# Kernel optimization log

Hardware: AMD Instinct MI355X
Metric: run time of the kernel (lower is better)

Reference implementation:

```python
import jax, jax.numpy as jnp
import numpy as np

POOL, D_MODEL, D_FF, M_DIM = 512, 1024, 4096, 64
B, S, K = 2, 2048, 8


def setup_inputs() -> dict:
    key = jax.random.key(0)
    ks = jax.random.split(key, 8)
    x = jax.random.normal(ks[0], (B, S, D_MODEL), dtype=jnp.float32)
    selected_indices = jax.random.randint(ks[1], (B, S, K), 0, POOL, dtype=jnp.int32)
    pattern_weights = jax.random.normal(ks[2], (B, S, K), dtype=jnp.float32)
    base_patterns = 0.02 * jax.random.normal(ks[3], (POOL, D_FF), dtype=jnp.float32)
    # nn.Linear(d_model, pool_size*mod_dim): weight [P*M, d_model], xavier-uniform
    lim_cm = float(np.sqrt(6.0 / (D_MODEL + POOL * M_DIM)))
    cm_w = jax.random.uniform(ks[4], (POOL * M_DIM, D_MODEL), jnp.float32, -lim_cm, lim_cm)
    cm_b = jnp.zeros((POOL * M_DIM,), jnp.float32)
    adj_proj = 0.01 * jax.random.normal(ks[5], (M_DIM, D_FF), dtype=jnp.float32)
    lim_w2 = float(np.sqrt(6.0 / (D_FF + D_MODEL)))
    w2_w = jax.random.uniform(ks[6], (D_MODEL, D_FF), jnp.float32, -lim_w2, lim_w2)
    w2_b = jnp.zeros((D_MODEL,), jnp.float32)
    return {"x": x, "selected_indices": selected_indices, "pattern_weights": pattern_weights,
            "base_patterns": base_patterns, "cm_w": cm_w, "cm_b": cm_b,
            "adj_proj": adj_proj, "w2_w": w2_w, "w2_b": w2_b}


def reference(x, selected_indices, pattern_weights, base_patterns, cm_w, cm_b, adj_proj, w2_w, w2_b):
    b, s, k = selected_indices.shape
    # gather base firing patterns for selected neurons: [b,s,k,d_ff]
    bp = base_patterns[selected_indices]
    # dense context modulation then gather (matches original module): [b,s,P,M]
    mod = (jnp.einsum('bsd,nd->bsn', x, cm_w) + cm_b).reshape(b, s, POOL, M_DIM)
    sel_mod = jnp.take_along_axis(mod, selected_indices[..., None], axis=2)  # [b,s,k,M]
    adjustments = jnp.einsum('bskm,mf->bskf', sel_mod, adj_proj)
    adjusted = bp + adjustments  # [b,s,k,d_ff]
    w = jax.nn.softmax(pattern_weights, axis=-1)
    combined = jnp.einsum('bsk,bskf->bsf', w, adjusted)  # [b,s,d_ff]
    activated = jax.nn.gelu(combined, approximate=False)  # torch default gelu = exact erf
    return jnp.einsum('bsf,df->bsd', activated, w2_w) + w2_b
```

## Files before the change

### kernel.cpp

```cpp
#include <hip/hip_runtime.h>
#include <math.h>

#define T_    4096
#define K_    8
#define POOL_ 512
#define DM_   1024
#define DFF_  4096
#define MD_   64
#define KC_   576
#define NSPLIT 4
#define NCAP  256

typedef __bf16 bf16x8 __attribute__((ext_vector_type(8)));
typedef __bf16 bf16x4 __attribute__((ext_vector_type(4)));
typedef float  f32x4  __attribute__((ext_vector_type(4)));

typedef __attribute__((address_space(1))) const void g_void;
typedef __attribute__((address_space(3))) void s_void;

__device__ __forceinline__ void async_ld16(const void* g, void* s) {
    __builtin_amdgcn_global_load_lds((g_void*)g, (s_void*)s, 16, 0, 0);
}
__device__ __forceinline__ float gelu_exact(float g) {
    return 0.5f * g * (1.f + erff(g * 0.70710678118654752f));
}
__device__ __forceinline__ bf16x4 cvt4(float4 v) {
    bf16x4 o;
    o[0] = (__bf16)v.x; o[1] = (__bf16)v.y; o[2] = (__bf16)v.z; o[3] = (__bf16)v.w;
    return o;
}

__global__ __launch_bounds__(256) void k_hist(const int* __restrict__ sel,
                                              int* __restrict__ counts) {
    int i = blockIdx.x * 256 + threadIdx.x;
    if (i < T_ * K_) atomicAdd(&counts[sel[i]], 1);
}

__global__ __launch_bounds__(512) void k_scan(const int* __restrict__ counts,
                                              int* __restrict__ offsets,
                                              int* __restrict__ cursor) {
    __shared__ int s[512];
    const int t = threadIdx.x;
    const int c = counts[t];
    s[t] = c;
    __syncthreads();
    for (int d = 1; d < 512; d <<= 1) {
        int v = (t >= d) ? s[t - d] : 0;
        __syncthreads();
        s[t] += v;
        __syncthreads();
    }
    offsets[t] = s[t] - c;
    cursor[t]  = s[t] - c;
    if (t == 511) offsets[512] = s[511];
}

__global__ __launch_bounds__(256) void k_scatter(const int* __restrict__ sel,
                                                 int* __restrict__ cursor,
                                                 int* __restrict__ bucket,
                                                 int* __restrict__ rank) {
    int i = blockIdx.x * 256 + threadIdx.x;
    if (i < T_ * K_) {
        int p = sel[i];
        int pos = atomicAdd(&cursor[p], 1);
        bucket[pos] = i;
        rank[i] = pos;
    }
}

__global__ __launch_bounds__(256, 8) void k_selmod(
    const float* __restrict__ x, const float* __restrict__ cm_w,
    const int* __restrict__ bucket, const int* __restrict__ offsets,
    float* __restrict__ Yp)
{
    const int p     = blockIdx.x;
    const int slice = blockIdx.y;
    const int tid   = threadIdx.x;
    __shared__ int list[NCAP];
    __shared__ __align__(16) __bf16 Xl[64][72];
    __shared__ __align__(16) __bf16 Wl[64][72];

    const int off = offsets[p];
    const int n   = min(offsets[p + 1] - off, NCAP);
    if (n == 0) return;
    for (int i = tid; i < n; i += 256) list[i] = bucket[off + i] >> 3;
    __syncthreads();

    const int wave = tid >> 6, lane = tid & 63, quad = lane >> 4, l15 = lane & 15;
    const int srow = tid >> 3;
    const int part = tid & 7;
    const int k0   = slice * (DM_ / NSPLIT);

    const float* w0 = cm_w + (long)(p * 64 + srow)      * DM_ + k0;
    const float* w1 = cm_w + (long)(p * 64 + srow + 32) * DM_ + k0;
    float* Yo = Yp + (long)slice * ((long)T_ * K_ * MD_);

    for (int base = 0; base < n; base += 64) {
        f32x4 acc[4] = {};
        int li0 = base + srow;      if (li0 >= n) li0 = n - 1;
        int li1 = base + srow + 32; if (li1 >= n) li1 = n - 1;
        const float* x0 = x + (long)list[li0] * DM_ + k0;
        const float* x1 = x + (long)list[li1] * DM_ + k0;

        for (int kc = 0; kc < DM_ / NSPLIT; kc += 64) {
            #pragma unroll
            for (int u = 0; u < 2; ++u) {
                const int c = kc + u * 32 + part * 4;
                float4 a0 = *(const float4*)(x0 + c);
                float4 a1 = *(const float4*)(x1 + c);
                float4 b0 = *(const float4*)(w0 + c);
                float4 b1 = *(const float4*)(w1 + c);
                const int lc = u * 32 + part * 4;
                *(bf16x4*)&Xl[srow     ][lc] = cvt4(a0);
                *(bf16x4*)&Xl[srow + 32][lc] = cvt4(a1);
                *(bf16x4*)&Wl[srow     ][lc] = cvt4(b0);
                *(bf16x4*)&Wl[srow + 32][lc] = cvt4(b1);
            }
            __syncthreads();
            #pragma unroll
            for (int ks = 0; ks < 2; ++ks) {
                const int ko = ks * 32 + quad * 8;
                bf16x8 bfr = *(const bf16x8*)&Wl[wave * 16 + l15][ko];
                #pragma unroll
                for (int i = 0; i < 4; ++i) {
                    bf16x8 afr = *(const bf16x8*)&Xl[i * 16 + l15][ko];
                    acc[i] = __builtin_amdgcn_mfma_f32_16x16x32_bf16(afr, bfr, acc[i], 0, 0, 0);
                }
            }
            __syncthreads();
        }
        const int mcol = wave * 16 + l15;
        #pragma unroll
        for (int i = 0; i < 4; ++i) {
            #pragma unroll
            for (int r = 0; r < 4; ++r) {
                int prow = base + i * 16 + quad * 4 + r;
                if (prow < n)
                    Yo[(long)(off + prow) * MD_ + mcol] = acc[i][r];
            }
        }
    }
}

__global__ __launch_bounds__(256) void k_wdense(
    const float* __restrict__ Yp, const int* __restrict__ sel,
    const int* __restrict__ rank, const float* __restrict__ pw,
    const float* __restrict__ cm_b, __bf16* __restrict__ Wd)
{
    const int tid = threadIdx.x;
    const int tt = tid >> 6, m = tid & 63;
    const int t = blockIdx.x * 4 + tt;
    __shared__ float w_s[4][8];
    __shared__ int   sidx[4][8];
    __shared__ int   rnk[4][8];
    __shared__ __align__(16) __bf16 row[4][KC_];

    if (m < 8) {
        w_s[tt][m]  = pw[t * 8 + m];
        sidx[tt][m] = sel[t * 8 + m];
        rnk[tt][m]  = rank[t * 8 + m];
    }
    __syncthreads();
    if (m == 0) {
        float mx = w_s[tt][0];
        #pragma unroll
        for (int k = 1; k < 8; ++k) mx = fmaxf(mx, w_s[tt][k]);
        float sum = 0.f;
        #pragma unroll
        for (int k = 0; k < 8; ++k) { float e = expf(w_s[tt][k] - mx); w_s[tt][k] = e; sum += e; }
        float inv = 1.f / sum;
        #pragma unroll
        for (int k = 0; k < 8; ++k) w_s[tt][k] *= inv;
    }
    __syncthreads();
    *(uint4*)&row[tt][m * 8] = make_uint4(0, 0, 0, 0);
    {
        const long YN = (long)T_ * K_ * MD_;
        float a = 0.f;
        #pragma unroll
        for (int k = 0; k < 8; ++k) {
            const long base = (long)rnk[tt][k] * MD_ + m;
            float y = cm_b[sidx[tt][k] * 64 + m];
            #pragma unroll
            for (int s = 0; s < NSPLIT; ++s) y += Yp[s * YN + base];
            a += w_s[tt][k] * y;
        }
        row[tt][512 + m] = (__bf16)a;
    }
    __syncthreads();
    if (m == 0) {
        #pragma unroll
        for (int k = 0; k < 8; ++k) {
            int c = sidx[tt][k];
            row[tt][c] = (__bf16)((float)row[tt][c] + w_s[tt][k]);
        }
    }
    __syncthreads();
    const uint4* src = (const uint4*)&row[0][0];
    uint4* dst = (uint4*)(Wd + (long)blockIdx.x * 4 * KC_);
    for (int e = tid; e < 4 * KC_ * 2 / 16; e += 256) dst[e] = src[e];
}

__global__ __launch_bounds__(256) void k_buildP(
    const float* __restrict__ bp, const float* __restrict__ adj,
    __bf16* __restrict__ P)
{
    __shared__ __bf16 tile[64][72];
    const int tid = threadIdx.x;
    const int bx = blockIdx.x, f0 = blockIdx.y * 64;
    const float* src = (bx < 8) ? (bp + (long)bx * 64 * DFF_) : adj;
    for (int e = tid; e < 4096; e += 256) {
        int f = e & 63, c = e >> 6;
        tile[c][f] = (__bf16)src[(long)c * DFF_ + f0 + f];
    }
    __syncthreads();
    const int c0 = bx * 64;
    for (int e = tid; e < 4096; e += 256) {
        int c = e & 63, f = e >> 6;
        P[(long)(f0 + f) * KC_ + c0 + c] = tile[c][f];
    }
}

__global__ __launch_bounds__(256) void k_cvt(const float* __restrict__ src,
                                             __bf16* __restrict__ dst, int n16) {
    int i = blockIdx.x * 256 + threadIdx.x;
    if (i >= n16) return;
    const float4* s = (const float4*)src + (long)i * 4;
    float4 a = s[0], b = s[1], c = s[2], d = s[3];
    bf16x8 o0, o1;
    o0[0]=(__bf16)a.x; o0[1]=(__bf16)a.y; o0[2]=(__bf16)a.z; o0[3]=(__bf16)a.w;
    o0[4]=(__bf16)b.x; o0[5]=(__bf16)b.y; o0[6]=(__bf16)b.z; o0[7]=(__bf16)b.w;
    o1[0]=(__bf16)c.x; o1[1]=(__bf16)c.y; o1[2]=(__bf16)c.z; o1[3]=(__bf16)c.w;
    o1[4]=(__bf16)d.x; o1[5]=(__bf16)d.y; o1[6]=(__bf16)d.z; o1[7]=(__bf16)d.w;
    bf16x8* dp = (bf16x8*)dst + (long)i * 2;
    dp[0] = o0; dp[1] = o1;
}

__global__ __launch_bounds__(256) void k_actgemm(
    const __bf16* __restrict__ A, const __bf16* __restrict__ Bw,
    __bf16* __restrict__ act)
{
    __shared__ __align__(16) __bf16 sA[128 * 32];
    __shared__ __align__(16) __bf16 sB[128 * 32];
    const int tid  = threadIdx.x;
    const int tm   = blockIdx.y * 128, tn = blockIdx.x * 128;
    const int wave = tid >> 6, lane = tid & 63, quad = lane >> 4, l15 = lane & 15;
    const int wm   = (wave >> 1) * 64, wn = (wave & 1) * 64;

    f32x4 acc[4][4] = {};

    const int e    = tid * 8;
    const int srow = e >> 5;
    const int scol = e & 31;
    const __bf16* agp0 = A  + ((long)(tm + srow)      * KC_ + scol);
    const __bf16* agp1 = A  + ((long)(tm + 64 + srow) * KC_ + scol);
    const __bf16* bgp0 = Bw + ((long)(tn + srow)      * KC_ + scol);
    const __bf16* bgp1 = Bw + ((long)(tn + 64 + srow) * KC_ + scol);
    void* sa0 = (void*)(sA + e);
    void* sa1 = (void*)(sA + 2048 + e);
    void* sb0 = (void*)(sB + e);
    void* sb1 = (void*)(sB + 2048 + e);

    for (int kk = 0; kk < KC_; kk += 32) {
        async_ld16(agp0 + kk, sa0);
        async_ld16(agp1 + kk, sa1);
        async_ld16(bgp0 + kk, sb0);
        async_ld16(bgp1 + kk, sb1);
        __syncthreads();
        bf16x8 af[4], bf[4];
        #pragma unroll
        for (int i = 0; i < 4; ++i)
            af[i] = *(const bf16x8*)(sA + (wm + i * 16 + l15) * 32 + quad * 8);
        #pragma unroll
        for (int j = 0; j < 4; ++j)
            bf[j] = *(const bf16x8*)(sB + (wn + j * 16 + l15) * 32 + quad * 8);
        #pragma unroll
        for (int i = 0; i < 4; ++i)
            #pragma unroll
            for (int j = 0; j < 4; ++j)
                acc[i][j] = __builtin_amdgcn_mfma_f32_16x16x32_bf16(af[i], bf[j], acc[i][j], 0, 0, 0);
        __syncthreads();
    }

    #pragma unroll
    for (int j = 0; j < 4; ++j) {
        const int col = tn + wn + j * 16 + l15;
        #pragma unroll
        for (int i = 0; i < 4; ++i) {
            const int row = tm + wm + i * 16 + quad * 4;
            #pragma unroll
            for (int r = 0; r < 4; ++r)
                act[(long)(row + r) * DFF_ + col] = (__bf16)gelu_exact(acc[i][j][r]);
        }
    }
}

__global__ __launch_bounds__(256) void k_outgemm(
    const __bf16* __restrict__ A, const __bf16* __restrict__ Bw,
    const float* __restrict__ bias, float* __restrict__ out)
{
    __shared__ __align__(16) __bf16 sA[128 * 128];
    __shared__ __align__(16) __bf16 sB[128 * 128];
    const int tid  = threadIdx.x;
    const int tm   = blockIdx.y * 128, tn = blockIdx.x * 128;
    const int wave = tid >> 6, lane = tid & 63, quad = lane >> 4, l15 = lane & 15;
    const int wm   = (wave >> 1) * 64, wn = (wave & 1) * 64;

    f32x4 acc[4][4] = {};

    const int e  = tid * 8;
    const int r0 = e >> 5;
    const int cc = e & 31;

    for (int kk = 0; kk < DFF_; kk += 128) {
        #pragma unroll
        for (int s = 0; s < 4; ++s) {
            #pragma unroll
            for (int q = 0; q < 2; ++q) {
                async_ld16(A  + (long)(tm + q * 64 + r0) * DFF_ + kk + s * 32 + cc,
                           (void*)(sA + s * 4096 + q * 2048 + e));
                async_ld16(Bw + (long)(tn + q * 64 + r0) * DFF_ + kk + s * 32 + cc,
                           (void*)(sB + s * 4096 + q * 2048 + e));
            }
        }
        __syncthreads();
        #pragma unroll
        for (int s = 0; s < 4; ++s) {
            bf16x8 af[4], bf[4];
            #pragma unroll
            for (int i = 0; i < 4; ++i)
                af[i] = *(const bf16x8*)(sA + s * 4096 + (wm + i * 16 + l15) * 32 + quad * 8);
            #pragma unroll
            for (int j = 0; j < 4; ++j)
                bf[j] = *(const bf16x8*)(sB + s * 4096 + (wn + j * 16 + l15) * 32 + quad * 8);
            #pragma unroll
            for (int i = 0; i < 4; ++i)
                #pragma unroll
                for (int j = 0; j < 4; ++j)
                    acc[i][j] = __builtin_amdgcn_mfma_f32_16x16x32_bf16(af[i], bf[j], acc[i][j], 0, 0, 0);
        }
        __syncthreads();
    }

    #pragma unroll
    for (int j = 0; j < 4; ++j) {
        const int col = tn + wn + j * 16 + l15;
        const float bj = bias[col];
        #pragma unroll
        for (int i = 0; i < 4; ++i) {
            const int row = tm + wm + i * 16 + quad * 4;
            #pragma unroll
            for (int r = 0; r < 4; ++r)
                out[(long)(row + r) * 1024 + col] = acc[i][j][r] + bj;
        }
    }
}

extern "C" void kernel_launch(void* const* d_in, const int* in_sizes, int n_in,
                              void* d_out, int out_size, void* d_ws, size_t ws_size,
                              hipStream_t stream) {
    const float* x    = (const float*)d_in[0];
    const int*   sel  = (const int*)  d_in[1];
    const float* pw   = (const float*)d_in[2];
    const float* bp   = (const float*)d_in[3];
    const float* cm_w = (const float*)d_in[4];
    const float* cm_b = (const float*)d_in[5];
    const float* adj  = (const float*)d_in[6];
    const float* w2   = (const float*)d_in[7];
    const float* w2b  = (const float*)d_in[8];
    float* out = (float*)d_out;

    char* ws = (char*)d_ws;
    float*  Yp   = (float*)ws;
    __bf16* act  = (__bf16*)ws;
    __bf16* P    = (__bf16*)(ws + (size_t)32 * 1024 * 1024);
    __bf16* w2bf = (__bf16*)(ws + (size_t)37 * 1024 * 1024);
    char*  bins  = ws + (size_t)45 * 1024 * 1024;
    int* bucket  = (int*)bins;
    int* rank    = (int*)(bins + 131072);
    int* counts  = (int*)(bins + 262144);
    int* cursor  = (int*)(bins + 264192);
    int* offsets = (int*)(bins + 266240);

    __bf16* Wd = (__bf16*)d_out;

    hipMemsetAsync(counts, 0, 4096, stream);
    k_hist   <<<128, 256, 0, stream>>>(sel, counts);
    k_scan   <<<1,   512, 0, stream>>>(counts, offsets, cursor);
    k_scatter<<<128, 256, 0, stream>>>(sel, cursor, bucket, rank);
    k_selmod <<<dim3(POOL_, NSPLIT), 256, 0, stream>>>(x, cm_w, bucket, offsets, Yp);
    k_wdense <<<T_ / 4, 256, 0, stream>>>(Yp, sel, rank, pw, cm_b, Wd);
    k_buildP <<<dim3(9, 64), 256, 0, stream>>>(bp, adj, P);
    k_cvt    <<<1024, 256, 0, stream>>>(w2, w2bf, DM_ * DFF_ / 16);
    k_actgemm<<<dim3(DFF_ / 128, T_ / 128), 256, 0, stream>>>(Wd, P, act);
    k_outgemm<<<dim3(DM_ / 128, T_ / 128), 256, 0, stream>>>(act, w2bf, w2b, out);
}
```

Before: 417.5 us.

## Split selmod over output columns with full-K weight tile and prequantized bf16 x

Converts x to bf16 once in a separate pass, then restructures the context-modulation GEMM so each block owns 16 of the 64 output columns for a pool entry. The block caches that full 16x1024 weight slice in LDS and walks all of K, which removes the four-way K-split partial sums and their reduction in k_wdense. The intent is to cut fp32 x reads and the extra Yp traffic. The cost is an extra conversion kernel and each x row being gathered four times, once per column slice, and each block now does only one MFMA chain per k-step. Y now lives in the output buffer, and Wd is moved to an offset inside it.

```diff
diff --git a/kernel.cpp b/kernel.cpp
--- a/kernel.cpp
+++ b/kernel.cpp
@@ -8,7 +8,6 @@
 #define DFF_  4096
 #define MD_   64
 #define KC_   576
-#define NSPLIT 4
 #define NCAP  256
 
 typedef __bf16 bf16x8 __attribute__((ext_vector_type(8)));
@@ -65,159 +64,6 @@
         int pos = atomicAdd(&cursor[p], 1);
         bucket[pos] = i;
         rank[i] = pos;
-    }
-}
-
-__global__ __launch_bounds__(256, 8) void k_selmod(
-    const float* __restrict__ x, const float* __restrict__ cm_w,
-    const int* __restrict__ bucket, const int* __restrict__ offsets,
-    float* __restrict__ Yp)
-{
-    const int p     = blockIdx.x;
-    const int slice = blockIdx.y;
-    const int tid   = threadIdx.x;
-    __shared__ int list[NCAP];
-    __shared__ __align__(16) __bf16 Xl[64][72];
-    __shared__ __align__(16) __bf16 Wl[64][72];
-
-    const int off = offsets[p];
-    const int n   = min(offsets[p + 1] - off, NCAP);
-    if (n == 0) return;
-    for (int i = tid; i < n; i += 256) list[i] = bucket[off + i] >> 3;
-    __syncthreads();
-
-    const int wave = tid >> 6, lane = tid & 63, quad = lane >> 4, l15 = lane & 15;
-    const int srow = tid >> 3;
-    const int part = tid & 7;
-    const int k0   = slice * (DM_ / NSPLIT);
-
-    const float* w0 = cm_w + (long)(p * 64 + srow)      * DM_ + k0;
-    const float* w1 = cm_w + (long)(p * 64 + srow + 32) * DM_ + k0;
-    float* Yo = Yp + (long)slice * ((long)T_ * K_ * MD_);
-
-    for (int base = 0; base < n; base += 64) {
-        f32x4 acc[4] = {};
-        int li0 = base + srow;      if (li0 >= n) li0 = n - 1;
-        int li1 = base + srow + 32; if (li1 >= n) li1 = n - 1;
-        const float* x0 = x + (long)list[li0] * DM_ + k0;
-        const float* x1 = x + (long)list[li1] * DM_ + k0;
-
-        for (int kc = 0; kc < DM_ / NSPLIT; kc += 64) {
-            #pragma unroll
-            for (int u = 0; u < 2; ++u) {
-                const int c = kc + u * 32 + part * 4;
-                float4 a0 = *(const float4*)(x0 + c);
-                float4 a1 = *(const float4*)(x1 + c);
-                float4 b0 = *(const float4*)(w0 + c);
-                float4 b1 = *(const float4*)(w1 + c);
-                const int lc = u * 32 + part * 4;
-                *(bf16x4*)&Xl[srow     ][lc] = cvt4(a0);
-                *(bf16x4*)&Xl[srow + 32][lc] = cvt4(a1);
-                *(bf16x4*)&Wl[srow     ][lc] = cvt4(b0);
-                *(bf16x4*)&Wl[srow + 32][lc] = cvt4(b1);
-            }
-            __syncthreads();
-            #pragma unroll
-            for (int ks = 0; ks < 2; ++ks) {
-                const int ko = ks * 32 + quad * 8;
-                bf16x8 bfr = *(const bf16x8*)&Wl[wave * 16 + l15][ko];
-                #pragma unroll
-                for (int i = 0; i < 4; ++i) {
-                    bf16x8 afr = *(const bf16x8*)&Xl[i * 16 + l15][ko];
-                    acc[i] = __builtin_amdgcn_mfma_f32_16x16x32_bf16(afr, bfr, acc[i], 0, 0, 0);
-                }
-            }
-            __syncthreads();
-        }
-        const int mcol = wave * 16 + l15;
-        #pragma unroll
-        for (int i = 0; i < 4; ++i) {
-            #pragma unroll
-            for (int r = 0; r < 4; ++r) {
-                int prow = base + i * 16 + quad * 4 + r;
-                if (prow < n)
-                    Yo[(long)(off + prow) * MD_ + mcol] = acc[i][r];
-            }
-        }
-    }
-}
-
-__global__ __launch_bounds__(256) void k_wdense(
-    const float* __restrict__ Yp, const int* __restrict__ sel,
-    const int* __restrict__ rank, const float* __restrict__ pw,
-    const float* __restrict__ cm_b, __bf16* __restrict__ Wd)
-{
-    const int tid = threadIdx.x;
-    const int tt = tid >> 6, m = tid & 63;
-    const int t = blockIdx.x * 4 + tt;
-    __shared__ float w_s[4][8];
-    __shared__ int   sidx[4][8];
-    __shared__ int   rnk[4][8];
-    __shared__ __align__(16) __bf16 row[4][KC_];
-
-    if (m < 8) {
-        w_s[tt][m]  = pw[t * 8 + m];
-        sidx[tt][m] = sel[t * 8 + m];
-        rnk[tt][m]  = rank[t * 8 + m];
-    }
-    __syncthreads();
-    if (m == 0) {
-        float mx = w_s[tt][0];
-        #pragma unroll
-        for (int k = 1; k < 8; ++k) mx = fmaxf(mx, w_s[tt][k]);
-        float sum = 0.f;
-        #pragma unroll
-        for (int k = 0; k < 8; ++k) { float e = expf(w_s[tt][k] - mx); w_s[tt][k] = e; sum += e; }
-        float inv = 1.f / sum;
-        #pragma unroll
-        for (int k = 0; k < 8; ++k) w_s[tt][k] *= inv;
-    }
-    __syncthreads();
-    *(uint4*)&row[tt][m * 8] = make_uint4(0, 0, 0, 0);
-    {
-        const long YN = (long)T_ * K_ * MD_;
-        float a = 0.f;
-        #pragma unroll
-        for (int k = 0; k < 8; ++k) {
-            const long base = (long)rnk[tt][k] * MD_ + m;
-            float y = cm_b[sidx[tt][k] * 64 + m];
-            #pragma unroll
-            for (int s = 0; s < NSPLIT; ++s) y += Yp[s * YN + base];
-            a += w_s[tt][k] * y;
-        }
-        row[tt][512 + m] = (__bf16)a;
-    }
-    __syncthreads();
-    if (m == 0) {
-        #pragma unroll
-        for (int k = 0; k < 8; ++k) {
-            int c = sidx[tt][k];
-            row[tt][c] = (__bf16)((float)row[tt][c] + w_s[tt][k]);
-        }
-    }
-    __syncthreads();
-    const uint4* src = (const uint4*)&row[0][0];
-    uint4* dst = (uint4*)(Wd + (long)blockIdx.x * 4 * KC_);
-    for (int e = tid; e < 4 * KC_ * 2 / 16; e += 256) dst[e] = src[e];
-}
-
-__global__ __launch_bounds__(256) void k_buildP(
-    const float* __restrict__ bp, const float* __restrict__ adj,
-    __bf16* __restrict__ P)
-{
-    __shared__ __bf16 tile[64][72];
-    const int tid = threadIdx.x;
-    const int bx = blockIdx.x, f0 = blockIdx.y * 64;
-    const float* src = (bx < 8) ? (bp + (long)bx * 64 * DFF_) : adj;
-    for (int e = tid; e < 4096; e += 256) {
-        int f = e & 63, c = e >> 6;
-        tile[c][f] = (__bf16)src[(long)c * DFF_ + f0 + f];
-    }
-    __syncthreads();
-    const int c0 = bx * 64;
-    for (int e = tid; e < 4096; e += 256) {
-        int c = e & 63, f = e >> 6;
-        P[(long)(f0 + f) * KC_ + c0 + c] = tile[c][f];
     }
 }
 
@@ -236,6 +82,143 @@
     dp[0] = o0; dp[1] = o1;
 }
 
+__global__ __launch_bounds__(256) void k_selmod(
+    const __bf16* __restrict__ xb, const float* __restrict__ cm_w,
+    const int* __restrict__ bucket, const int* __restrict__ offsets,
+    float* __restrict__ Y)
+{
+    const int p   = blockIdx.x;
+    const int ms  = blockIdx.y;
+    const int tid = threadIdx.x;
+    __shared__ int list[NCAP];
+    __shared__ __align__(16) __bf16 Wl[16][1032];
+    __shared__ __align__(16) __bf16 Xl[64][72];
+
+    const int off = offsets[p];
+    const int n   = min(offsets[p + 1] - off, NCAP);
+    if (n == 0) return;
+    for (int i = tid; i < n; i += 256) list[i] = bucket[off + i] >> 3;
+
+    {
+        const int wr = tid >> 4;
+        const int wl = tid & 15;
+        const float* wsrc = cm_w + (long)(p * 64 + ms * 16 + wr) * DM_;
+        #pragma unroll
+        for (int j = 0; j < 16; ++j) {
+            float4 v = *(const float4*)(wsrc + j * 64 + wl * 4);
+            *(bf16x4*)&Wl[wr][j * 64 + wl * 4] = cvt4(v);
+        }
+    }
+    __syncthreads();
+
+    const int wave = tid >> 6, lane = tid & 63, quad = lane >> 4, l15 = lane & 15;
+    const int srow = tid >> 3;
+    const int part = tid & 7;
+
+    for (int base = 0; base < n; base += 64) {
+        f32x4 acc = {};
+        int li0 = base + srow;      if (li0 >= n) li0 = n - 1;
+        int li1 = base + srow + 32; if (li1 >= n) li1 = n - 1;
+        const __bf16* x0 = xb + (long)list[li0] * DM_ + part * 8;
+        const __bf16* x1 = xb + (long)list[li1] * DM_ + part * 8;
+
+        for (int kc = 0; kc < DM_; kc += 64) {
+            *(bf16x8*)&Xl[srow     ][part * 8] = *(const bf16x8*)(x0 + kc);
+            *(bf16x8*)&Xl[srow + 32][part * 8] = *(const bf16x8*)(x1 + kc);
+            __syncthreads();
+            #pragma unroll
+            for (int ks = 0; ks < 2; ++ks) {
+                const int ko = ks * 32 + quad * 8;
+                bf16x8 bfr = *(const bf16x8*)&Wl[l15][kc + ko];
+                bf16x8 afr = *(const bf16x8*)&Xl[wave * 16 + l15][ko];
+                acc = __builtin_amdgcn_mfma_f32_16x16x32_bf16(afr, bfr, acc, 0, 0, 0);
+            }
+            __syncthreads();
+        }
+        #pragma unroll
+        for (int r = 0; r < 4; ++r) {
+            int prow = base + wave * 16 + quad * 4 + r;
+            if (prow < n)
+                Y[(long)(off + prow) * MD_ + ms * 16 + l15] = acc[r];
+        }
+    }
+}
+
+__global__ __launch_bounds__(256) void k_wdense(
+    const float* __restrict__ Y, const int* __restrict__ sel,
+    const int* __restrict__ rank, const float* __restrict__ pw,
+    const float* __restrict__ cm_b, __bf16* __restrict__ Wd)
+{
+    const int tid = threadIdx.x;
+    const int tt = tid >> 6, m = tid & 63;
+    const int t = blockIdx.x * 4 + tt;
+    __shared__ float w_s[4][8];
+    __shared__ int   sidx[4][8];
+    __shared__ int   rnk[4][8];
+    __shared__ __align__(16) __bf16 row[4][KC_];
+
+    if (m < 8) {
+        w_s[tt][m]  = pw[t * 8 + m];
+        sidx[tt][m] = sel[t * 8 + m];
+        rnk[tt][m]  = rank[t * 8 + m];
+    }
+    __syncthreads();
+    if (m == 0) {
+        float mx = w_s[tt][0];
+        #pragma unroll
+        for (int k = 1; k < 8; ++k) mx = fmaxf(mx, w_s[tt][k]);
+        float sum = 0.f;
+        #pragma unroll
+        for (int k = 0; k < 8; ++k) { float e = expf(w_s[tt][k] - mx); w_s[tt][k] = e; sum += e; }
+        float inv = 1.f / sum;
+        #pragma unroll
+        for (int k = 0; k < 8; ++k) w_s[tt][k] *= inv;
+    }
+    __syncthreads();
+    *(uint4*)&row[tt][m * 8] = make_uint4(0, 0, 0, 0);
+    {
+        float a = 0.f;
+        #pragma unroll
+        for (int k = 0; k < 8; ++k) {
+            float y = cm_b[sidx[tt][k] * 64 + m] + Y[(long)rnk[tt][k] * MD_ + m];
+            a += w_s[tt][k] * y;
+        }
+        row[tt][512 + m] = (__bf16)a;
+    }
+    __syncthreads();
+    if (m == 0) {
+        #pragma unroll
+        for (int k = 0; k < 8; ++k) {
+            int c = sidx[tt][k];
+            row[tt][c] = (__bf16)((float)row[tt][c] + w_s[tt][k]);
+        }
+    }
+    __syncthreads();
+    const uint4* src = (const uint4*)&row[0][0];
+    uint4* dst = (uint4*)(Wd + (long)blockIdx.x * 4 * KC_);
+    for (int e = tid; e < 4 * KC_ * 2 / 16; e += 256) dst[e] = src[e];
+}
+
+__global__ __launch_bounds__(256) void k_buildP(
+    const float* __restrict__ bp, const float* __restrict__ adj,
+    __bf16* __restrict__ P)
+{
+    __shared__ __bf16 tile[64][72];
+    const int tid = threadIdx.x;
+    const int bx = blockIdx.x, f0 = blockIdx.y * 64;
+    const float* src = (bx < 8) ? (bp + (long)bx * 64 * DFF_) : adj;
+    for (int e = tid; e < 4096; e += 256) {
+        int f = e & 63, c = e >> 6;
+        tile[c][f] = (__bf16)src[(long)c * DFF_ + f0 + f];
+    }
+    __syncthreads();
+    const int c0 = bx * 64;
+    for (int e = tid; e < 4096; e += 256) {
+        int c = e & 63, f = e >> 6;
+        P[(long)(f0 + f) * KC_ + c0 + c] = tile[c][f];
+    }
+}
+
 __global__ __launch_bounds__(256) void k_actgemm(
     const __bf16* __restrict__ A, const __bf16* __restrict__ Bw,
     __bf16* __restrict__ act)
@@ -371,7 +354,7 @@
     float* out = (float*)d_out;
 
     char* ws = (char*)d_ws;
-    float*  Yp   = (float*)ws;
+    __bf16* x_bf = (__bf16*)ws;
     __bf16* act  = (__bf16*)ws;
     __bf16* P    = (__bf16*)(ws + (size_t)32 * 1024 * 1024);
     __bf16* w2bf = (__bf16*)(ws + (size_t)37 * 1024 * 1024);
@@ -382,14 +365,16 @@
     int* cursor  = (int*)(bins + 264192);
     int* offsets = (int*)(bins + 266240);
 
-    __bf16* Wd = (__bf16*)d_out;
+    float*  Y  = (float*)d_out;
+    __bf16* Wd = (__bf16*)((char*)d_out + (size_t)8 * 1024 * 1024);
 
     hipMemsetAsync(counts, 0, 4096, stream);
     k_hist   <<<128, 256, 0, stream>>>(sel, counts);
     k_scan   <<<1,   512, 0, stream>>>(counts, offsets, cursor);
     k_scatter<<<128, 256, 0, stream>>>(sel, cursor, bucket, rank);
-    k_selmod <<<dim3(POOL_, NSPLIT), 256, 0, stream>>>(x, cm_w, bucket, offsets, Yp);
-    k_wdense <<<T_ / 4, 256, 0, stream>>>(Yp, sel, rank, pw, cm_b, Wd);
+    k_cvt    <<<1024, 256, 0, stream>>>(x, x_bf, T_ * DM_ / 16);
+    k_selmod <<<dim3(POOL_, 4), 256, 0, stream>>>(x_bf, cm_w, bucket, offsets, Y);
+    k_wdense <<<T_ / 4, 256, 0, stream>>>(Y, sel, rank, pw, cm_b, Wd);
     k_buildP <<<dim3(9, 64), 256, 0, stream>>>(bp, adj, P);
     k_cvt    <<<1024, 256, 0, stream>>>(w2, w2bf, DM_ * DFF_ / 16);
     k_actgemm<<<dim3(DFF_ / 128, T_ / 128), 256, 0, stream>>>(Wd, P, act);
```

Result: no change. 414.9 us (-0.6%).
